# Kernel tuning notes

Hardware: AMD Instinct MI355X
Metric: run time of the kernel (lower is better)

The kernel has to match this reference:

```python
import jax, jax.numpy as jnp
import numpy as np

DEPTH = 6
N_LEAF = 2 ** DEPTH          # 64
GATE_COUNT = N_LEAF - 1      # 63
B = 1024
GATING_FEATURES = 512
IN_FEATURES = 512
OUT_FEATURES = 512


def setup_inputs() -> dict:
    key = jax.random.key(0)
    k1, k2, k3, k4 = jax.random.split(key, 4)
    x_gating = jax.random.normal(k1, (B, GATING_FEATURES), dtype=jnp.float32)
    x_leaf = jax.random.normal(k2, (B, IN_FEATURES), dtype=jnp.float32)
    # kaiming-normal-ish init scales
    gw = jax.random.normal(k3, (GATING_FEATURES, GATE_COUNT), dtype=jnp.float32) * (1.0 / np.sqrt(GATING_FEATURES))
    gb = jnp.zeros((GATE_COUNT,), dtype=jnp.float32)
    pw = jax.random.normal(k4, (OUT_FEATURES, IN_FEATURES, N_LEAF), dtype=jnp.float32) * (1.0 / np.sqrt(IN_FEATURES))
    pb = jnp.zeros((OUT_FEATURES, N_LEAF), dtype=jnp.float32)
    return {"x_gating": x_gating, "x_leaf": x_leaf, "gw": gw, "gb": gb, "pw": pw, "pb": pb}


def _leaf_probs(x_gating, gw, gb):
    # gatings: (B, gate_count), internal nodes in breadth-first order
    gatings = jax.nn.sigmoid(x_gating @ gw + gb)
    b = gatings.shape[0]
    dens = jnp.ones((b, 1), dtype=gatings.dtype)  # root density
    start = 0
    for d in range(DEPTH):
        n_par = 2 ** d
        g = gatings[:, start:start + n_par]          # (B, n_par)
        # left child (even it+1) gets g, right child gets 1-g, interleaved
        dens = jnp.stack([dens * g, dens * (1.0 - g)], axis=-1).reshape(b, 2 * n_par)
        start += n_par
    return dens  # (B, n_leaf) = leaf densities (last n_leaf node densities)


def reference(x_gating, x_leaf, gw, gb, pw, pb):
    leaf_probs = _leaf_probs(x_gating, gw, gb)              # (B, L)
    # gated projection applied to x_leaf, summed over leaves:
    # equals ((pw @ leaf_probs.T).permute(2,0,1) @ x_leaf[...,None])[...,0]
    result = jnp.einsum('oil,bl,bi->bo', pw, leaf_probs, x_leaf)
    result = result + leaf_probs @ pb.T                     # gated bias (B, O)
    return result
```

## Files before the change

kernel.cpp:

```cpp
#include <hip/hip_runtime.h>
#include <hip/hip_bf16.h>
#include <stdint.h>

#define B_SZ   1024
#define GF     512
#define GC     63
#define NLEAF  64
#define IN_F   512
#define OUT_F  512

typedef float f32x4 __attribute__((ext_vector_type(4)));
typedef __bf16 bf16x8 __attribute__((ext_vector_type(8)));

struct alignas(16) BV8 { __hip_bfloat162 a, b, c, d; };
union PK8 { BV8 v; bf16x8 f; };
union BU { __hip_bfloat162 h; unsigned int u; };

__device__ inline void pack8(const float* f, __hip_bfloat16* dst) {
  BU a, b, c, d;
  a.h = __float22bfloat162_rn(make_float2(f[0], f[1]));
  b.h = __float22bfloat162_rn(make_float2(f[2], f[3]));
  c.h = __float22bfloat162_rn(make_float2(f[4], f[5]));
  d.h = __float22bfloat162_rn(make_float2(f[6], f[7]));
  *(uint4*)dst = make_uint4(a.u, b.u, c.u, d.u);
}

__global__ __launch_bounds__(512, 2) void k_leafprobs(
    const float* __restrict__ xg, const float* __restrict__ gw,
    const float* __restrict__ gb, float* __restrict__ p_ws)
{
  __shared__ float xsr[GF];
  __shared__ float part[512];
  __shared__ float gates[GC + 1];
  const int b = blockIdx.x;
  const int t = threadIdx.x;

  xsr[t] = xg[(size_t)b * GF + t];
  __syncthreads();

  const int ks = t >> 6, g = t & 63;
  float acc = 0.f;
  if (g < GC) {
    const float* gp = gw + (size_t)(ks * 64) * GC + g;
    const float* xp = &xsr[ks * 64];
#pragma unroll 8
    for (int k = 0; k < 64; ++k) acc += xp[k] * gp[(size_t)k * GC];
  }
  part[t] = acc;
  __syncthreads();

  if (t < GC) {
    float s = gb[t];
#pragma unroll
    for (int r = 0; r < 8; ++r) s += part[r * 64 + t];
    gates[t] = 1.f / (1.f + expf(-s));
  }
  __syncthreads();

  if (t < NLEAF) {
    float v = 1.f;
    int idx = 0, start = 0;
#pragma unroll
    for (int d = 0; d < 6; ++d) {
      int bit = (t >> (5 - d)) & 1;
      float gg = gates[start + idx];
      v *= bit ? (1.f - gg) : gg;
      idx = 2 * idx + bit;
      start += (1 << d);
    }
    p_ws[(size_t)b * NLEAF + t] = v;
  }
}

#define SK 16
#define KI 32

template <bool ATOMIC>
__global__ __launch_bounds__(256, 2) void k_fused(
    const float* __restrict__ x_leaf,
    const float* __restrict__ p_ws,
    const float* __restrict__ pw,
    float* __restrict__ dst)
{
  __shared__ __align__(16) float           xs[256][KI + 4];
  __shared__ __align__(16) __hip_bfloat16  bs[2][64 * 72];

  const int tid  = threadIdx.x;
  const int lane = tid & 63;
  const int wid  = tid >> 6;
  const int quad = lane >> 4;
  const int l15  = lane & 15;

  const int bid = blockIdx.x;
  const int nt  = bid & 7;
  const int mt  = (bid >> 3) & 3;
  const int kc  = bid >> 5;

  const int row_m0 = mt * 256;
  const int o0     = nt * 64;
  const int i0     = kc * KI;
  const int wm     = wid * 64;

  {
    const float* src = x_leaf + (size_t)(row_m0 + tid) * IN_F + i0;
#pragma unroll
    for (int q = 0; q < KI / 4; ++q)
      *(float4*)&xs[tid][q * 4] = *(const float4*)(src + q * 4);
  }

  f32x4 pr[4][2][2];
#pragma unroll
  for (int mi = 0; mi < 4; ++mi) {
    int row = row_m0 + wm + mi * 16 + l15;
#pragma unroll
    for (int ks = 0; ks < 2; ++ks) {
      const f32x4* src = (const f32x4*)(p_ws + (size_t)row * NLEAF + ks * 32 + quad * 8);
      pr[mi][ks][0] = src[0];
      pr[mi][ks][1] = src[1];
    }
  }
  {
    float sink = 0.f;
#pragma unroll
    for (int mi = 0; mi < 4; ++mi)
#pragma unroll
      for (int ks = 0; ks < 2; ++ks)
#pragma unroll
        for (int h = 0; h < 2; ++h) {
          f32x4 v = pr[mi][ks][h];
          sink += v.x + v.y + v.z + v.w;
        }
    if (sink == 1.2345678e37f) xs[0][0] = sink;
  }

  const int br  = tid >> 2;
  const int seg = tid & 3;
  const float* bsrc0 = pw + ((size_t)(o0 + br) * IN_F + i0) * NLEAF + seg * 16;

  f32x4 acc[4][4];
#pragma unroll
  for (int mi = 0; mi < 4; ++mi)
#pragma unroll
    for (int ni = 0; ni < 4; ++ni)
      acc[mi][ni] = (f32x4)(0.f);

  float4 rb[2][4];

#define BLOAD(T, BUF)                                                         \
  {                                                                           \
    const float4* s_ = (const float4*)(bsrc0 + (size_t)(T) * NLEAF);          \
    rb[BUF][0] = s_[0]; rb[BUF][1] = s_[1];                                   \
    rb[BUF][2] = s_[2]; rb[BUF][3] = s_[3];                                   \
  }

  BLOAD(0, 0)
  BLOAD(1, 1)

#pragma unroll 2
  for (int it = 0; it < KI; ++it) {
    const int buf = it & 1;

    {
      float f[16];
      *(float4*)&f[0]  = rb[buf][0];
      *(float4*)&f[4]  = rb[buf][1];
      *(float4*)&f[8]  = rb[buf][2];
      *(float4*)&f[12] = rb[buf][3];
      __hip_bfloat16* d = &bs[buf][br * 72 + seg * 16];
      pack8(&f[0], d);
      pack8(&f[8], d + 8);
    }

    if (it + 2 < KI) BLOAD(it + 2, buf)

    __syncthreads();

    float xv[4];
#pragma unroll
    for (int mi = 0; mi < 4; ++mi) xv[mi] = xs[wm + mi * 16 + l15][it];

    const __hip_bfloat16* bsc = &bs[buf][0];
#pragma unroll
    for (int ks = 0; ks < 2; ++ks) {
      bf16x8 af[4];
#pragma unroll
      for (int mi = 0; mi < 4; ++mi) {
        f32x4 lo = pr[mi][ks][0] * xv[mi];
        f32x4 hi = pr[mi][ks][1] * xv[mi];
        PK8 u;
        u.v.a = __float22bfloat162_rn(make_float2(lo.x, lo.y));
        u.v.b = __float22bfloat162_rn(make_float2(lo.z, lo.w));
        u.v.c = __float22bfloat162_rn(make_float2(hi.x, hi.y));
        u.v.d = __float22bfloat162_rn(make_float2(hi.z, hi.w));
        af[mi] = u.f;
      }
#pragma unroll
      for (int ni = 0; ni < 4; ++ni) {
        bf16x8 bfr = *(const bf16x8*)&bsc[(ni * 16 + l15) * 72 + ks * 32 + quad * 8];
#pragma unroll
        for (int mi = 0; mi < 4; ++mi)
          acc[mi][ni] = __builtin_amdgcn_mfma_f32_16x16x32_bf16(
              af[mi], bfr, acc[mi][ni], 0, 0, 0);
      }
    }
  }
#undef BLOAD

#pragma unroll
  for (int mi = 0; mi < 4; ++mi) {
#pragma unroll
    for (int ni = 0; ni < 4; ++ni) {
      int row = row_m0 + wm + mi * 16 + quad * 4;
      int col = o0 + ni * 16 + l15;
      if (ATOMIC) {
        float* o = dst + (size_t)row * OUT_F + col;
        atomicAdd(o,             acc[mi][ni][0]);
        atomicAdd(o + OUT_F,     acc[mi][ni][1]);
        atomicAdd(o + 2 * OUT_F, acc[mi][ni][2]);
        atomicAdd(o + 3 * OUT_F, acc[mi][ni][3]);
      } else {
        float* o = dst + ((size_t)kc << 19) + (size_t)row * OUT_F + col;
        o[0]         = acc[mi][ni][0];
        o[OUT_F]     = acc[mi][ni][1];
        o[2 * OUT_F] = acc[mi][ni][2];
        o[3 * OUT_F] = acc[mi][ni][3];
      }
    }
  }
}

__global__ __launch_bounds__(256, 4) void k_reduce(
    const float* __restrict__ parts, const float* __restrict__ p_ws,
    const float* __restrict__ pb, float* __restrict__ out, int nparts)
{
  __shared__ float ps_l[2 * NLEAF];
  const int t  = threadIdx.x;
  const int b0 = blockIdx.x * 2;

  if (t < 32)
    ((f32x4*)ps_l)[t] = ((const f32x4*)(p_ws + (size_t)b0 * NLEAF))[t];
  __syncthreads();

  const int row = b0 + (t >> 7);
  const int c0  = (t & 127) * 4;
  const f32x4* ps = (const f32x4*)&ps_l[(t >> 7) * NLEAF];

  f32x4 a;
#pragma unroll
  for (int jo = 0; jo < 4; ++jo) {
    const f32x4* pbo = (const f32x4*)(pb + (size_t)(c0 + jo) * NLEAF);
    f32x4 s = (f32x4)(0.f);
#pragma unroll
    for (int lv = 0; lv < 16; ++lv) s += pbo[lv] * ps[lv];
    a[jo] = s.x + s.y + s.z + s.w;
  }

#pragma unroll 8
  for (int k = 0; k < nparts; ++k)
    a += *(const f32x4*)(parts + ((size_t)k << 19) + (size_t)row * OUT_F + c0);

  *(f32x4*)(out + (size_t)row * OUT_F + c0) = a;
}

extern "C" void kernel_launch(void* const* d_in, const int* in_sizes, int n_in,
                              void* d_out, int out_size, void* d_ws, size_t ws_size,
                              hipStream_t stream) {
  const float* xg = (const float*)d_in[0];
  const float* xl = (const float*)d_in[1];
  const float* gw = (const float*)d_in[2];
  const float* gb = (const float*)d_in[3];
  const float* pw = (const float*)d_in[4];
  const float* pb = (const float*)d_in[5];
  float* out = (float*)d_out;

  const size_t P_BYTES = (size_t)B_SZ * NLEAF * 4;
  const size_t SLICE   = (size_t)B_SZ * OUT_F * 4;

  float* p_ws  = (float*)d_ws;
  float* parts = (float*)((char*)d_ws + P_BYTES);

  k_leafprobs<<<dim3(B_SZ), dim3(512), 0, stream>>>(xg, gw, gb, p_ws);

  if (ws_size >= P_BYTES + SK * SLICE) {
    k_fused<false><<<dim3(512), dim3(256), 0, stream>>>(xl, p_ws, pw, parts);
    k_reduce<<<dim3(512), dim3(256), 0, stream>>>(parts, p_ws, pb, out, SK);
  } else {
    k_reduce<<<dim3(512), dim3(256), 0, stream>>>(parts, p_ws, pb, out, 0);
    k_fused<true><<<dim3(512), dim3(256), 0, stream>>>(xl, p_ws, pw, out);
  }
}
```

Baseline: 170.0 us.

## Use 512-thread blocks with single-barrier double-buffered B staging in fused kernel

```diff
diff --git a/kernel.cpp b/kernel.cpp
--- a/kernel.cpp
+++ b/kernel.cpp
@@ -76,13 +76,13 @@
 #define KI 32
 
 template <bool ATOMIC>
-__global__ __launch_bounds__(256, 2) void k_fused(
+__global__ __launch_bounds__(512, 4) void k_fused(
     const float* __restrict__ x_leaf,
     const float* __restrict__ p_ws,
     const float* __restrict__ pw,
     float* __restrict__ dst)
 {
-  __shared__ __align__(16) float           xs[256][KI + 4];
+  __shared__ __align__(16) float           xs[KI][256];
   __shared__ __align__(16) __hip_bfloat16  bs[2][64 * 72];
 
   const int tid  = threadIdx.x;
@@ -99,19 +99,25 @@
   const int row_m0 = mt * 256;
   const int o0     = nt * 64;
   const int i0     = kc * KI;
-  const int wm     = wid * 64;
+  const int wm     = wid * 32;
 
   {
-    const float* src = x_leaf + (size_t)(row_m0 + tid) * IN_F + i0;
-#pragma unroll
-    for (int q = 0; q < KI / 4; ++q)
-      *(float4*)&xs[tid][q * 4] = *(const float4*)(src + q * 4);
-  }
-
-  f32x4 pr[4][2][2];
-#pragma unroll
-  for (int mi = 0; mi < 4; ++mi) {
-    int row = row_m0 + wm + mi * 16 + l15;
+    const int r = tid & 255;
+    const int h = tid >> 8;
+    const float4* src = (const float4*)(x_leaf + (size_t)(row_m0 + r) * IN_F + i0 + h * 16);
+#pragma unroll
+    for (int q = 0; q < 4; ++q) {
+      float4 v = src[q];
+      const int c = h * 16 + q * 4;
+      xs[c + 0][r] = v.x; xs[c + 1][r] = v.y;
+      xs[c + 2][r] = v.z; xs[c + 3][r] = v.w;
+    }
+  }
+
+  f32x4 pr[2][2][2];
+#pragma unroll
+  for (int mi = 0; mi < 2; ++mi) {
+    const int row = row_m0 + wm + mi * 16 + l15;
 #pragma unroll
     for (int ks = 0; ks < 2; ++ks) {
       const f32x4* src = (const f32x4*)(p_ws + (size_t)row * NLEAF + ks * 32 + quad * 8);
@@ -119,72 +125,62 @@
       pr[mi][ks][1] = src[1];
     }
   }
-  {
-    float sink = 0.f;
-#pragma unroll
-    for (int mi = 0; mi < 4; ++mi)
-#pragma unroll
-      for (int ks = 0; ks < 2; ++ks)
-#pragma unroll
-        for (int h = 0; h < 2; ++h) {
-          f32x4 v = pr[mi][ks][h];
-          sink += v.x + v.y + v.z + v.w;
-        }
-    if (sink == 1.2345678e37f) xs[0][0] = sink;
-  }
-
-  const int br  = tid >> 2;
-  const int seg = tid & 3;
-  const float* bsrc0 = pw + ((size_t)(o0 + br) * IN_F + i0) * NLEAF + seg * 16;
-
-  f32x4 acc[4][4];
-#pragma unroll
-  for (int mi = 0; mi < 4; ++mi)
+
+  const int br  = tid >> 3;
+  const int seg = tid & 7;
+  const float* bsrc0 = pw + ((size_t)(o0 + br) * IN_F + i0) * NLEAF + seg * 8;
+
+  f32x4 acc[2][4];
+#pragma unroll
+  for (int mi = 0; mi < 2; ++mi)
 #pragma unroll
     for (int ni = 0; ni < 4; ++ni)
       acc[mi][ni] = (f32x4)(0.f);
 
-  float4 rb[2][4];
+  float4 rb[2][2];
 
 #define BLOAD(T, BUF)                                                         \
   {                                                                           \
     const float4* s_ = (const float4*)(bsrc0 + (size_t)(T) * NLEAF);          \
     rb[BUF][0] = s_[0]; rb[BUF][1] = s_[1];                                   \
-    rb[BUF][2] = s_[2]; rb[BUF][3] = s_[3];                                   \
-  }
+  }
+
+#define BSTAGE(BUF)                                                           \
+  {                                                                           \
+    float f_[8];                                                              \
+    *(float4*)&f_[0] = rb[BUF][0];                                            \
+    *(float4*)&f_[4] = rb[BUF][1];                                            \
+    pack8(f_, &bs[BUF][br * 72 + seg * 8]);                                   \
+  }
+
+#define BARRIER() asm volatile("s_waitcnt lgkmcnt(0)\n\ts_barrier" ::: "memory")
 
   BLOAD(0, 0)
   BLOAD(1, 1)
+  BSTAGE(0)
+  BLOAD(2, 0)
+  BARRIER();
 
 #pragma unroll 2
   for (int it = 0; it < KI; ++it) {
     const int buf = it & 1;
 
-    {
-      float f[16];
-      *(float4*)&f[0]  = rb[buf][0];
-      *(float4*)&f[4]  = rb[buf][1];
-      *(float4*)&f[8]  = rb[buf][2];
-      *(float4*)&f[12] = rb[buf][3];
-      __hip_bfloat16* d = &bs[buf][br * 72 + seg * 16];
-      pack8(&f[0], d);
-      pack8(&f[8], d + 8);
-    }
-
-    if (it + 2 < KI) BLOAD(it + 2, buf)
-
-    __syncthreads();
-
-    float xv[4];
-#pragma unroll
-    for (int mi = 0; mi < 4; ++mi) xv[mi] = xs[wm + mi * 16 + l15][it];
+    if (it + 1 < KI) {
+      BSTAGE(buf ^ 1)
+      if (it + 3 < KI) BLOAD(it + 3, buf ^ 1)
+    }
+
+    float xv[2];
+    xv[0] = xs[it][wm + l15];
+    xv[1] = xs[it][wm + 16 + l15];
 
     const __hip_bfloat16* bsc = &bs[buf][0];
+    __builtin_amdgcn_s_setprio(1);
 #pragma unroll
     for (int ks = 0; ks < 2; ++ks) {
-      bf16x8 af[4];
-#pragma unroll
-      for (int mi = 0; mi < 4; ++mi) {
+      bf16x8 af[2];
+#pragma unroll
+      for (int mi = 0; mi < 2; ++mi) {
         f32x4 lo = pr[mi][ks][0] * xv[mi];
         f32x4 hi = pr[mi][ks][1] * xv[mi];
         PK8 u;
@@ -198,16 +194,21 @@
       for (int ni = 0; ni < 4; ++ni) {
         bf16x8 bfr = *(const bf16x8*)&bsc[(ni * 16 + l15) * 72 + ks * 32 + quad * 8];
 #pragma unroll
-        for (int mi = 0; mi < 4; ++mi)
+        for (int mi = 0; mi < 2; ++mi)
           acc[mi][ni] = __builtin_amdgcn_mfma_f32_16x16x32_bf16(
               af[mi], bfr, acc[mi][ni], 0, 0, 0);
       }
     }
+    __builtin_amdgcn_s_setprio(0);
+
+    BARRIER();
   }
 #undef BLOAD
-
-#pragma unroll
-  for (int mi = 0; mi < 4; ++mi) {
+#undef BSTAGE
+#undef BARRIER
+
+#pragma unroll
+  for (int mi = 0; mi < 2; ++mi) {
 #pragma unroll
     for (int ni = 0; ni < 4; ++ni) {
       int row = row_m0 + wm + mi * 16 + quad * 4;
@@ -282,10 +283,10 @@
   k_leafprobs<<<dim3(B_SZ), dim3(512), 0, stream>>>(xg, gw, gb, p_ws);
 
   if (ws_size >= P_BYTES + SK * SLICE) {
-    k_fused<false><<<dim3(512), dim3(256), 0, stream>>>(xl, p_ws, pw, parts);
+    k_fused<false><<<dim3(512), dim3(512), 0, stream>>>(xl, p_ws, pw, parts);
     k_reduce<<<dim3(512), dim3(256), 0, stream>>>(parts, p_ws, pb, out, SK);
   } else {
     k_reduce<<<dim3(512), dim3(256), 0, stream>>>(parts, p_ws, pb, out, 0);
-    k_fused<true><<<dim3(512), dim3(256), 0, stream>>>(xl, p_ws, pw, out);
-  }
-}
+    k_fused<true><<<dim3(512), dim3(512), 0, stream>>>(xl, p_ws, pw, out);
+  }
+}
```

Measured after the change: 171.1 us. Within noise of the previous version (+0.6%).

## Switch fused GEMM to fp16 MFMA with deeper prefetch and swizzled LDS

Applied to the files above, without the earlier changes.

```diff
diff --git a/kernel.cpp b/kernel.cpp
--- a/kernel.cpp
+++ b/kernel.cpp
@@ -1,5 +1,4 @@
 #include <hip/hip_runtime.h>
-#include <hip/hip_bf16.h>
 #include <stdint.h>
 
 #define B_SZ   1024
@@ -10,19 +9,16 @@
 #define OUT_F  512
 
 typedef float f32x4 __attribute__((ext_vector_type(4)));
-typedef __bf16 bf16x8 __attribute__((ext_vector_type(8)));
-
-struct alignas(16) BV8 { __hip_bfloat162 a, b, c, d; };
-union PK8 { BV8 v; bf16x8 f; };
-union BU { __hip_bfloat162 h; unsigned int u; };
-
-__device__ inline void pack8(const float* f, __hip_bfloat16* dst) {
-  BU a, b, c, d;
-  a.h = __float22bfloat162_rn(make_float2(f[0], f[1]));
-  b.h = __float22bfloat162_rn(make_float2(f[2], f[3]));
-  c.h = __float22bfloat162_rn(make_float2(f[4], f[5]));
-  d.h = __float22bfloat162_rn(make_float2(f[6], f[7]));
-  *(uint4*)dst = make_uint4(a.u, b.u, c.u, d.u);
+typedef __fp16 h16x2 __attribute__((ext_vector_type(2)));
+typedef __fp16 h16x8 __attribute__((ext_vector_type(8)));
+typedef _Float16 f16x2 __attribute__((ext_vector_type(2)));
+
+union HF8 { f16x2 h2[4]; h16x8 v; uint4 u; };
+
+__device__ inline f16x2 pkrtz(float a, float b) {
+  union { h16x2 r; f16x2 f; } u;
+  u.r = __builtin_amdgcn_cvt_pkrtz(a, b);
+  return u.f;
 }
 
 __global__ __launch_bounds__(512, 2) void k_leafprobs(
@@ -82,14 +78,15 @@
     const float* __restrict__ pw,
     float* __restrict__ dst)
 {
-  __shared__ __align__(16) float           xs[256][KI + 4];
-  __shared__ __align__(16) __hip_bfloat16  bs[2][64 * 72];
+  __shared__ __align__(16) float         xs[KI][256];
+  __shared__ __align__(16) unsigned char bs8[2 * 8192];
 
   const int tid  = threadIdx.x;
   const int lane = tid & 63;
   const int wid  = tid >> 6;
   const int quad = lane >> 4;
   const int l15  = lane & 15;
+  const int l7   = l15 & 7;
 
   const int bid = blockIdx.x;
   const int nt  = bid & 7;
@@ -104,39 +101,43 @@
   {
     const float* src = x_leaf + (size_t)(row_m0 + tid) * IN_F + i0;
 #pragma unroll
-    for (int q = 0; q < KI / 4; ++q)
-      *(float4*)&xs[tid][q * 4] = *(const float4*)(src + q * 4);
-  }
-
-  f32x4 pr[4][2][2];
+    for (int q = 0; q < 8; ++q) {
+      float4 v = *(const float4*)(src + q * 4);
+      xs[q * 4 + 0][tid] = v.x;
+      xs[q * 4 + 1][tid] = v.y;
+      xs[q * 4 + 2][tid] = v.z;
+      xs[q * 4 + 3][tid] = v.w;
+    }
+  }
+
+  HF8 prh[4][2];
 #pragma unroll
   for (int mi = 0; mi < 4; ++mi) {
-    int row = row_m0 + wm + mi * 16 + l15;
+    const int row = row_m0 + wm + mi * 16 + l15;
 #pragma unroll
     for (int ks = 0; ks < 2; ++ks) {
       const f32x4* src = (const f32x4*)(p_ws + (size_t)row * NLEAF + ks * 32 + quad * 8);
-      pr[mi][ks][0] = src[0];
-      pr[mi][ks][1] = src[1];
+      f32x4 lo = src[0], hi = src[1];
+      prh[mi][ks].h2[0] = pkrtz(lo.x, lo.y);
+      prh[mi][ks].h2[1] = pkrtz(lo.z, lo.w);
+      prh[mi][ks].h2[2] = pkrtz(hi.x, hi.y);
+      prh[mi][ks].h2[3] = pkrtz(hi.z, hi.w);
     }
-  }
-  {
-    float sink = 0.f;
-#pragma unroll
-    for (int mi = 0; mi < 4; ++mi)
-#pragma unroll
-      for (int ks = 0; ks < 2; ++ks)
-#pragma unroll
-        for (int h = 0; h < 2; ++h) {
-          f32x4 v = pr[mi][ks][h];
-          sink += v.x + v.y + v.z + v.w;
-        }
-    if (sink == 1.2345678e37f) xs[0][0] = sink;
   }
 
   const int br  = tid >> 2;
   const int seg = tid & 3;
   const float* bsrc0 = pw + ((size_t)(o0 + br) * IN_F + i0) * NLEAF + seg * 16;
 
+  const int wsw   = (br & 7) << 4;
+  const int woff0 = br * 128 + ((seg * 32) ^ wsw);
+  const int woff1 = br * 128 + ((seg * 32 + 16) ^ wsw);
+  int coff[2];
+#pragma unroll
+  for (int ks = 0; ks < 2; ++ks)
+    coff[ks] = (ks * 64 + quad * 16) ^ (l7 << 4);
+  const int rbase = l15 * 128;
+
   f32x4 acc[4][4];
 #pragma unroll
   for (int mi = 0; mi < 4; ++mi)
@@ -144,67 +145,88 @@
     for (int ni = 0; ni < 4; ++ni)
       acc[mi][ni] = (f32x4)(0.f);
 
-  float4 rb[2][4];
-
-#define BLOAD(T, BUF)                                                         \
+  float4 rb[4][4];
+
+#define BLOAD(T, SLOT)                                                        \
   {                                                                           \
     const float4* s_ = (const float4*)(bsrc0 + (size_t)(T) * NLEAF);          \
-    rb[BUF][0] = s_[0]; rb[BUF][1] = s_[1];                                   \
-    rb[BUF][2] = s_[2]; rb[BUF][3] = s_[3];                                   \
+    rb[SLOT][0] = s_[0]; rb[SLOT][1] = s_[1];                                 \
+    rb[SLOT][2] = s_[2]; rb[SLOT][3] = s_[3];                                 \
+  }
+
+#define BSTAGE(SLOT, BUF)                                                     \
+  {                                                                           \
+    HF8 c0_, c1_;                                                             \
+    float4 a0_ = rb[SLOT][0], a1_ = rb[SLOT][1];                              \
+    float4 a2_ = rb[SLOT][2], a3_ = rb[SLOT][3];                              \
+    c0_.h2[0] = pkrtz(a0_.x, a0_.y);                                          \
+    c0_.h2[1] = pkrtz(a0_.z, a0_.w);                                          \
+    c0_.h2[2] = pkrtz(a1_.x, a1_.y);                                          \
+    c0_.h2[3] = pkrtz(a1_.z, a1_.w);                                          \
+    c1_.h2[0] = pkrtz(a2_.x, a2_.y);                                          \
+    c1_.h2[1] = pkrtz(a2_.z, a2_.w);                                          \
+    c1_.h2[2] = pkrtz(a3_.x, a3_.y);                                          \
+    c1_.h2[3] = pkrtz(a3_.z, a3_.w);                                          \
+    *(uint4*)(bs8 + (BUF) * 8192 + woff0) = c0_.u;                            \
+    *(uint4*)(bs8 + (BUF) * 8192 + woff1) = c1_.u;                            \
+  }
+
+#define BARRIER() asm volatile("s_waitcnt lgkmcnt(0)\n\ts_barrier" ::: "memory")
+
+#define STEP(IT, BUF, SNX)                                                    \
+  {                                                                           \
+    float xvf[4];                                                             \
+    _Float16 xh[4];                                                           \
+    _Pragma("unroll")                                                         \
+    for (int mi = 0; mi < 4; ++mi) xvf[mi] = xs[(IT)][wm + mi * 16 + l15];    \
+    _Pragma("unroll")                                                         \
+    for (int mi = 0; mi < 4; ++mi) xh[mi] = (_Float16)xvf[mi];                \
+    const unsigned char* bsr_ = bs8 + (BUF) * 8192;                           \
+    __builtin_amdgcn_s_setprio(1);                                            \
+    _Pragma("unroll")                                                         \
+    for (int ks = 0; ks < 2; ++ks) {                                          \
+      h16x8 af[4];                                                            \
+      _Pragma("unroll")                                                       \
+      for (int mi = 0; mi < 4; ++mi) {                                        \
+        HF8 t_;                                                               \
+        f16x2 xp_; xp_[0] = xh[mi]; xp_[1] = xh[mi];                          \
+        _Pragma("unroll")                                                     \
+        for (int j = 0; j < 4; ++j) t_.h2[j] = prh[mi][ks].h2[j] * xp_;       \
+        af[mi] = t_.v;                                                        \
+      }                                                                       \
+      _Pragma("unroll")                                                       \
+      for (int ni = 0; ni < 4; ++ni) {                                        \
+        h16x8 bfr = *(const h16x8*)(bsr_ + ni * 2048 + rbase + coff[ks]);     \
+        _Pragma("unroll")                                                     \
+        for (int mi = 0; mi < 4; ++mi)                                        \
+          acc[mi][ni] = __builtin_amdgcn_mfma_f32_16x16x32_f16(               \
+              af[mi], bfr, acc[mi][ni], 0, 0, 0);                             \
+      }                                                                       \
+    }                                                                         \
+    __builtin_amdgcn_s_setprio(0);                                            \
+    if ((IT) + 1 < KI) { BSTAGE(SNX, (BUF) ^ 1) }                             \
+    if ((IT) + 5 < KI) { BLOAD((IT) + 5, SNX) }                               \
+    BARRIER();                                                                \
   }
 
   BLOAD(0, 0)
   BLOAD(1, 1)
-
-#pragma unroll 2
-  for (int it = 0; it < KI; ++it) {
-    const int buf = it & 1;
-
-    {
-      float f[16];
-      *(float4*)&f[0]  = rb[buf][0];
-      *(float4*)&f[4]  = rb[buf][1];
-      *(float4*)&f[8]  = rb[buf][2];
-      *(float4*)&f[12] = rb[buf][3];
-      __hip_bfloat16* d = &bs[buf][br * 72 + seg * 16];
-      pack8(&f[0], d);
-      pack8(&f[8], d + 8);
-    }
-
-    if (it + 2 < KI) BLOAD(it + 2, buf)
-
-    __syncthreads();
-
-    float xv[4];
-#pragma unroll
-    for (int mi = 0; mi < 4; ++mi) xv[mi] = xs[wm + mi * 16 + l15][it];
-
-    const __hip_bfloat16* bsc = &bs[buf][0];
-#pragma unroll
-    for (int ks = 0; ks < 2; ++ks) {
-      bf16x8 af[4];
-#pragma unroll
-      for (int mi = 0; mi < 4; ++mi) {
-        f32x4 lo = pr[mi][ks][0] * xv[mi];
-        f32x4 hi = pr[mi][ks][1] * xv[mi];
-        PK8 u;
-        u.v.a = __float22bfloat162_rn(make_float2(lo.x, lo.y));
-        u.v.b = __float22bfloat162_rn(make_float2(lo.z, lo.w));
-        u.v.c = __float22bfloat162_rn(make_float2(hi.x, hi.y));
-        u.v.d = __float22bfloat162_rn(make_float2(hi.z, hi.w));
-        af[mi] = u.f;
-      }
-#pragma unroll
-      for (int ni = 0; ni < 4; ++ni) {
-        bf16x8 bfr = *(const bf16x8*)&bsc[(ni * 16 + l15) * 72 + ks * 32 + quad * 8];
-#pragma unroll
-        for (int mi = 0; mi < 4; ++mi)
-          acc[mi][ni] = __builtin_amdgcn_mfma_f32_16x16x32_bf16(
-              af[mi], bfr, acc[mi][ni], 0, 0, 0);
-      }
-    }
+  BLOAD(2, 2)
+  BLOAD(3, 3)
+  BSTAGE(0, 0)
+  BLOAD(4, 0)
+  BARRIER();
+
+  for (int itb = 0; itb < KI; itb += 4) {
+    STEP(itb + 0, 0, 1)
+    STEP(itb + 1, 1, 2)
+    STEP(itb + 2, 0, 3)
+    STEP(itb + 3, 1, 0)
   }
 #undef BLOAD
+#undef BSTAGE
+#undef BARRIER
+#undef STEP
 
 #pragma unroll
   for (int mi = 0; mi < 4; ++mi) {
```

New measurement: 167.4 us. Within noise of the previous version (-1.5%).
